# Kernel optimization log

Hardware: AMD Instinct MI355X
Metric: run time of the kernel (lower is better)

The kernel has to match this reference:

```python
import jax, jax.numpy as jnp
import numpy as np

# ---- problem sizes ----
N_NEURONS = 1536
N_INPUTS = 768
BATCH = 32
T = 256
DT = 1.0  # ms per step
SURRGRAD_SCALE = 10.0

# ---- per-cell-type physiology (recurrent): 0=excitatory, 1=inhibitory ----
CELL_TAU_MEM = np.array([20.0, 10.0], np.float32)   # ms
CELL_THETA   = np.array([-50.0, -50.0], np.float32) # mV
CELL_URESET  = np.array([-65.0, -65.0], np.float32) # mV
CELL_EL      = np.array([-65.0, -65.0], np.float32) # mV
CELL_GL      = np.array([10.0, 10.0], np.float32)   # nS
CELL_TAUREF  = np.array([2.0, 1.0], np.float32)     # ms

# ---- synapse types: AMPA(pre=exc), NMDA(pre=exc), GABA_A(pre=inh) ----
SYN_CELL_ID   = np.array([0, 0, 1], np.int32)
SYN_TAU_RISE  = np.array([0.5, 2.0, 0.5], np.float32)
SYN_TAU_DECAY = np.array([2.0, 100.0, 5.0], np.float32)
SYN_EREV      = np.array([0.0, 0.0, -70.0], np.float32)
SYN_GBAR      = np.array([1.0, 0.5, 1.0], np.float32)

# ---- feedforward: single excitatory input type, single AMPA synapse ----
FF_TAU_RISE, FF_TAU_DECAY, FF_EREV, FF_GBAR = 0.5, 2.0, 0.0, 1.0


@jax.custom_vjp
def spike(v):
    # Heaviside spike with fast-sigmoid surrogate gradient
    return (v >= 0).astype(v.dtype)

def _spike_fwd(v):
    return spike(v), v

def _spike_bwd(v, g):
    return (g / (SURRGRAD_SCALE * jnp.abs(v) + 1.0) ** 2,)

spike.defvjp(_spike_fwd, _spike_bwd)


def setup_inputs() -> dict:
    key = jax.random.key(0)
    ks = jax.random.split(key, 6)
    input_spikes = (jax.random.uniform(ks[0], (BATCH, T, N_INPUTS)) < 0.05).astype(jnp.float32)
    weights = jax.random.normal(ks[1], (N_NEURONS, N_NEURONS), jnp.float32) * 0.05
    weights_FF = jax.random.normal(ks[2], (N_INPUTS, N_NEURONS), jnp.float32) * 0.05
    cell_type_indices = jax.random.randint(ks[3], (N_NEURONS,), 0, 2, jnp.int32)
    cell_type_indices_FF = jnp.zeros((N_INPUTS,), jnp.int32)
    scaling_factors = jax.random.uniform(ks[4], (2, 2), jnp.float32, 0.5, 1.5)
    scaling_factors_FF = jax.random.uniform(ks[5], (1, 2), jnp.float32, 0.5, 1.5)
    return {
        'input_spikes': input_spikes,
        'weights': weights,
        'weights_FF': weights_FF,
        'scaling_factors': scaling_factors,
        'scaling_factors_FF': scaling_factors_FF,
        'cell_type_indices': cell_type_indices,
        'cell_type_indices_FF': cell_type_indices_FF,
    }


def _simulate(input_spikes, weights, weights_FF, scaling_factors, scaling_factors_FF,
              cell_type_indices, cell_type_indices_FF):
    ct = cell_type_indices
    B = input_spikes.shape[0]

    # per-neuron physiology gathered by cell type
    tau_mem = jnp.asarray(CELL_TAU_MEM)[ct]
    theta = jnp.asarray(CELL_THETA)[ct]
    u_reset = jnp.asarray(CELL_URESET)[ct]
    e_l = jnp.asarray(CELL_EL)[ct]
    g_l = jnp.asarray(CELL_GL)[ct]
    ref_steps = jnp.asarray(CELL_TAUREF)[ct] / DT
    leak_coef = DT / (tau_mem * g_l)  # dt / C_m

    # effective weights: cell-type scaling + presynaptic synapse-type mask
    sf = scaling_factors[ct[:, None], ct[None, :]]            # (N, N)
    W = weights * sf
    pre_mask = (jnp.asarray(SYN_CELL_ID)[:, None] == ct[None, :]).astype(W.dtype)  # (S, N)
    Ws = W[None, :, :] * pre_mask[:, :, None]                  # (S, N, N)
    sfF = scaling_factors_FF[cell_type_indices_FF[:, None], ct[None, :]]
    WF = weights_FF * sfF                                      # (n_in, N)

    alpha_r = jnp.exp(-DT / jnp.asarray(SYN_TAU_RISE))[:, None, None]   # (S,1,1)
    alpha_d = jnp.exp(-DT / jnp.asarray(SYN_TAU_DECAY))[:, None, None]
    arF = jnp.exp(jnp.float32(-DT / FF_TAU_RISE))
    adF = jnp.exp(jnp.float32(-DT / FF_TAU_DECAY))
    gbar = jnp.asarray(SYN_GBAR)
    gbarE = jnp.asarray(SYN_GBAR * SYN_EREV)
    S = gbar.shape[0]

    U0 = jnp.broadcast_to(e_l, (B, N_NEURONS))
    carry0 = (U0,
              jnp.zeros((B, N_NEURONS), jnp.float32),       # previous spikes
              jnp.zeros((S, B, N_NEURONS), jnp.float32),    # x (rise)
              jnp.zeros((S, B, N_NEURONS), jnp.float32),    # g (decay)
              jnp.zeros((B, N_NEURONS), jnp.float32),       # x_FF
              jnp.zeros((B, N_NEURONS), jnp.float32),       # g_FF
              jnp.zeros((B, N_NEURONS), jnp.float32))       # refractory counter

    def step(carry, I_t):
        U, s_prev, x, g, xF, gF, ref = carry
        # dual-exponential conductance update per synapse type
        inp = jnp.einsum('bn,snm->sbm', s_prev, Ws)
        x = alpha_r * x + inp
        g = alpha_d * g + x
        xF = arF * xF + I_t @ WF
        gF = adF * gF + xF
        # conductance-based synaptic current: sum_s gbar_s * g_s * (E_s - U)
        gtot = jnp.einsum('s,sbn->bn', gbar, g) + FF_GBAR * gF
        gE = jnp.einsum('s,sbn->bn', gbarE, g) + (FF_GBAR * FF_EREV) * gF
        I_syn = gE - gtot * U
        # leaky membrane integration
        U_new = U + leak_coef * (g_l * (e_l - U) + I_syn)
        # refractory clamp
        in_ref = ref > 0
        U_new = jnp.where(in_ref, u_reset, U_new)
        ref = jnp.maximum(ref - 1.0, 0.0)
        # surrogate-gradient spike and reset
        s_new = spike(U_new - theta)
        U_out = jnp.where(s_new > 0, u_reset, U_new)
        ref = jnp.where(s_new > 0, ref_steps, ref)
        return (U_out, s_new, x, g, xF, gF, ref), (s_new, U_out)

    I_seq = jnp.transpose(input_spikes, (1, 0, 2))  # (T, B, n_in)
    _, (spk, volts) = jax.lax.scan(step, carry0, I_seq)
    return jnp.transpose(spk, (1, 0, 2)), jnp.transpose(volts, (1, 0, 2))


def reference(input_spikes, weights, weights_FF, scaling_factors, scaling_factors_FF,
              cell_type_indices, cell_type_indices_FF):
    return _simulate(input_spikes, weights, weights_FF, scaling_factors, scaling_factors_FF,
                     cell_type_indices, cell_type_indices_FF)
```

## Files before the change

### kernel.cpp

```cpp
#include <hip/hip_runtime.h>
#include <stdint.h>


__global__ __launch_bounds__(768) void snn_lif_kernel(
    const float* __restrict__ I,
    const float* __restrict__ W,
    const float* __restrict__ WF,
    const float* __restrict__ sf,
    const float* __restrict__ sfF,
    const int*   __restrict__ ct,
    float* __restrict__ out,
    uint64_t* __restrict__ recpub)
{
    const int tid = threadIdx.x;
    const int j   = blockIdx.x & 7;
    const int b   = blockIdx.x >> 3;
    const int wv  = tid >> 6;
    const int wl  = tid & 63;

    __shared__ uint32_t ent[3840];
    __shared__ float    partF[11][192];
    __shared__ float    part0[12][192];
    __shared__ float    part1[12][192];
    __shared__ uint32_t totals_sh;
    __shared__ uint32_t tF_sh;
    __shared__ uint32_t ctm32_sh[48];
    __shared__ uint64_t fmask_sh[12];

    for (int r = 0; r < 2; ++r) {
        int c = ct[r * 768 + tid];
        uint64_t bal = __ballot(c != 0);
        if (wl == 0) {
            ctm32_sh[r * 24 + wv * 2]     = (uint32_t)bal;
            ctm32_sh[r * 24 + wv * 2 + 1] = (uint32_t)(bal >> 32);
        }
    }
    __syncthreads();

    const int m = j * 192 + ((tid < 192) ? tid : 0);
    const int   myct = ct[m];
    const float s0m  = sf[myct];
    const float s1m  = sf[2 + myct];
    const float sFm  = sfF[myct];
    const float lc   = (myct == 0) ? (1.0f / 200.0f) : (1.0f / 100.0f);
    const float refsteps = (myct == 0) ? 2.0f : 1.0f;
    const float ar0 = expf(-1.0f / 0.5f),  ad0 = expf(-1.0f / 2.0f);
    const float ar1 = expf(-1.0f / 2.0f),  ad1 = expf(-1.0f / 100.0f);
    const float ar2 = expf(-1.0f / 0.5f),  ad2 = expf(-1.0f / 5.0f);
    const float arF = expf(-1.0f / 0.5f),  adF = expf(-1.0f / 2.0f);

    float U = -65.0f, refc = 0.0f;
    float x0 = 0, g0 = 0, x1 = 0, g1 = 0, x2 = 0, g2 = 0, xF = 0, gF = 0;

    const uint32_t ctw = (wl < 48) ? ctm32_sh[wl] : 0u;
    const int btbase = b * 256;
    const uint32_t colv = (uint32_t)(j * 48 + wl);

    {
        float iv0 = __builtin_nontemporal_load(&I[(uint32_t)btbase * 768u + (uint32_t)tid]);
        uint64_t fb = __ballot(iv0 > 0.5f);
        if (wl == 0) fmask_sh[wv] = fb;
    }
    __syncthreads();
    if (wv == 0) {
        uint64_t fm = 0; uint32_t cF = 0;
        if (wl < 12) { fm = fmask_sh[wl]; cF = __popcll(fm); }
        uint32_t incl = cF;
        #pragma unroll
        for (int d = 1; d < 64; d <<= 1) {
            uint32_t u = __shfl_up(incl, d, 64);
            if (wl >= d) incl += u;
        }
        if (wl == 11) tF_sh = incl;
        if (wl < 12) {
            uint32_t pF = 3072u + (incl - cF);
            const uint32_t lanebase = (uint32_t)wl * 64u * 1536u;
            while (fm) {
                const int bit = __builtin_ctzll(fm);
                fm &= fm - 1;
                ent[pF++] = lanebase + (uint32_t)bit * 1536u;
            }
        }
    }

    for (int t = 0; t < 256; ++t) {
        __syncthreads();

        float iv_next = 0.0f;
        if (t < 255)
            iv_next = __builtin_nontemporal_load(
                &I[(uint32_t)(btbase + t + 1) * 768u + (uint32_t)tid]);

        if (wv == 0) {
            uint32_t sm = 0;
            if (wl < 48 && t > 0) {
                const uint32_t fi = (uint32_t)(btbase + t - 1) * 48u + (uint32_t)wl;
                for (;;) {
                    uint64_t v = __hip_atomic_load(&recpub[fi], __ATOMIC_RELAXED,
                                                   __HIP_MEMORY_SCOPE_AGENT);
                    if ((uint32_t)(v >> 32) == (uint32_t)t) { sm = (uint32_t)v; break; }
                    __builtin_amdgcn_s_sleep(1);
                }
            }
            const uint32_t c0 = __popc(sm & ~ctw);
            const uint32_t c1 = __popc(sm & ctw);
            uint32_t pack = c0 | (c1 << 16);
            uint32_t incl = pack;
            #pragma unroll
            for (int d = 1; d < 64; d <<= 1) {
                uint32_t u = __shfl_up(incl, d, 64);
                if (wl >= d) incl += u;
            }
            const uint32_t excl = incl - pack;
            if (wl == 47) totals_sh = incl;
            if (wl < 48) {
                uint32_t p0 = excl & 0xFFFFu;
                uint32_t p1 = 1536u + (excl >> 16);
                uint32_t mm = sm;
                const uint32_t lanebase = (uint32_t)wl * 32u * 1536u;
                while (mm) {
                    const int bit = __builtin_ctz(mm);
                    mm &= mm - 1;
                    const uint32_t off = lanebase + (uint32_t)bit * 1536u;
                    if ((ctw >> bit) & 1u) ent[p1++] = off;
                    else                   ent[p0++] = off;
                }
            }
        } else if (wl < 48) {
            const uint32_t tF = tF_sh;
            float4 zF = make_float4(0.f, 0.f, 0.f, 0.f);
            #pragma unroll 4
            for (uint32_t i = (uint32_t)(wv - 1); i < tF; i += 11u) {
                const float4 w = ((const float4*)(WF + ent[3072u + i]))[colv];
                zF.x += w.x; zF.y += w.y; zF.z += w.z; zF.w += w.w;
            }
            *(float4*)&partF[wv - 1][wl * 4] = zF;
        }
        __syncthreads();

        const uint32_t tp = totals_sh;
        const uint32_t t0 = tp & 0xFFFFu;
        const uint32_t t1 = tp >> 16;
        if (wl < 48) {
            float4 z0 = make_float4(0.f, 0.f, 0.f, 0.f);
            float4 z1 = z0;
            #pragma unroll 8
            for (uint32_t i = (uint32_t)wv; i < t0; i += 12u) {
                const float4 w = ((const float4*)(W + ent[i]))[colv];
                z0.x += w.x; z0.y += w.y; z0.z += w.z; z0.w += w.w;
            }
            #pragma unroll 8
            for (uint32_t i = (uint32_t)wv; i < t1; i += 12u) {
                const float4 w = ((const float4*)(W + ent[1536u + i]))[colv];
                z1.x += w.x; z1.y += w.y; z1.z += w.z; z1.w += w.w;
            }
            *(float4*)&part0[wv][wl * 4] = z0;
            *(float4*)&part1[wv][wl * 4] = z1;
        }
        {
            uint64_t fb = __ballot(iv_next > 0.5f);
            if (wl == 0) fmask_sh[wv] = fb;
        }
        __syncthreads();

        if (tid < 192) {
            float z0s = 0.f, z1s = 0.f, zFs = 0.f;
            #pragma unroll
            for (int k = 0; k < 11; ++k) zFs += partF[k][tid];
            #pragma unroll
            for (int k = 0; k < 12; ++k) { z0s += part0[k][tid]; z1s += part1[k][tid]; }
            z0s *= s0m; z1s *= s1m; zFs *= sFm;
            x0 = ar0 * x0 + z0s;  g0 = ad0 * g0 + x0;
            x1 = ar1 * x1 + z0s;  g1 = ad1 * g1 + x1;
            x2 = ar2 * x2 + z1s;  g2 = ad2 * g2 + x2;
            xF = arF * xF + zFs;  gF = adF * gF + xF;
            const float gtot = g0 + 0.5f * g1 + g2 + gF;
            const float gE   = -70.0f * g2;
            const float Isyn = gE - gtot * U;
            float Un = U + lc * (10.0f * (-65.0f - U) + Isyn);
            if (refc > 0.0f) Un = -65.0f;
            refc = fmaxf(refc - 1.0f, 0.0f);
            const bool s = (Un - (-50.0f)) >= 0.0f;
            const uint64_t bal = __ballot(s);
            if (wl == 0 || wl == 32) {
                const uint32_t half = (wl == 0) ? (uint32_t)bal : (uint32_t)(bal >> 32);
                const uint32_t word = (uint32_t)(j * 6 + wv * 2) + (wl == 32 ? 1u : 0u);
                const uint32_t widx = (uint32_t)(btbase + t) * 48u + word;
                const uint64_t v = ((uint64_t)(uint32_t)(t + 1) << 32) | half;
                __hip_atomic_store(&recpub[widx], v, __ATOMIC_RELAXED,
                                   __HIP_MEMORY_SCOPE_AGENT);
            }
            const float Uo = s ? -65.0f : Un;
            refc = s ? refsteps : refc;
            U = Uo;
            const uint32_t oidx = (uint32_t)(btbase + t) * 1536u + (uint32_t)m;
            __builtin_nontemporal_store(s ? 1.0f : 0.0f, &out[oidx]);
            __builtin_nontemporal_store(Uo, &out[12582912u + oidx]);
        }
        if (wv == 0 && t < 255) {
            uint64_t fm = 0; uint32_t cF = 0;
            if (wl < 12) { fm = fmask_sh[wl]; cF = __popcll(fm); }
            uint32_t incl = cF;
            #pragma unroll
            for (int d = 1; d < 64; d <<= 1) {
                uint32_t u = __shfl_up(incl, d, 64);
                if (wl >= d) incl += u;
            }
            if (wl == 11) tF_sh = incl;
            if (wl < 12) {
                uint32_t pF = 3072u + (incl - cF);
                const uint32_t lanebase = (uint32_t)wl * 64u * 1536u;
                while (fm) {
                    const int bit = __builtin_ctzll(fm);
                    fm &= fm - 1;
                    ent[pF++] = lanebase + (uint32_t)bit * 1536u;
                }
            }
        }
    }
}

extern "C" void kernel_launch(void* const* d_in, const int* in_sizes, int n_in,
                              void* d_out, int out_size, void* d_ws, size_t ws_size,
                              hipStream_t stream) {
    const float* I   = (const float*)d_in[0];
    const float* W   = (const float*)d_in[1];
    const float* WF  = (const float*)d_in[2];
    const float* sf  = (const float*)d_in[3];
    const float* sfF = (const float*)d_in[4];
    const int*   ct  = (const int*)d_in[5];

    uint64_t* recpub = (uint64_t*)d_ws;

    snn_lif_kernel<<<dim3(256), dim3(768), 0, stream>>>(
        I, W, WF, sf, sfF, ct, (float*)d_out, recpub);
}
```

Measured before the change: 845.3 us.

## Split each batch across 16 blocks of 384 threads with 96 neurons each

Each block now owns 96 neurons instead of 192, so the launch grows to 512 blocks of 384 threads. Each wave splits into two 24-lane half-rows that take alternating sparse-entry phases. The block-to-(batch, slice) mapping interleaves the two halves of a batch across blockIdx ranges. The intent is to shorten per-step gather and accumulate work and to use more CUs for the latency-bound recurrent loop. The cost is twice as many blocks polling the cross-block spike flags, duplicated per-block spike list construction, and more blocks that must be co-resident for the spin-wait scheme to avoid deadlock.

```diff
diff --git a/kernel.cpp b/kernel.cpp
--- a/kernel.cpp
+++ b/kernel.cpp
@@ -2,7 +2,7 @@
 #include <stdint.h>
 
 
-__global__ __launch_bounds__(768) void snn_lif_kernel(
+__global__ __launch_bounds__(384) void snn_lif_kernel(
     const float* __restrict__ I,
     const float* __restrict__ W,
     const float* __restrict__ WF,
@@ -13,31 +13,34 @@
     uint64_t* __restrict__ recpub)
 {
     const int tid = threadIdx.x;
-    const int j   = blockIdx.x & 7;
-    const int b   = blockIdx.x >> 3;
+    const int x    = blockIdx.x & 7;
+    const int r    = blockIdx.x >> 3;
+    const int half = r >> 5;
+    const int j    = x + 8 * half;
+    const int b    = ((r & 31) + (half << 4)) & 31;
     const int wv  = tid >> 6;
     const int wl  = tid & 63;
 
     __shared__ uint32_t ent[3840];
-    __shared__ float    partF[11][192];
-    __shared__ float    part0[12][192];
-    __shared__ float    part1[12][192];
+    __shared__ float    partF[10][96];
+    __shared__ float    part0[12][96];
+    __shared__ float    part1[12][96];
     __shared__ uint32_t totals_sh;
     __shared__ uint32_t tF_sh;
     __shared__ uint32_t ctm32_sh[48];
     __shared__ uint64_t fmask_sh[12];
 
-    for (int r = 0; r < 2; ++r) {
-        int c = ct[r * 768 + tid];
+    for (int rr = 0; rr < 4; ++rr) {
+        int c = ct[rr * 384 + tid];
         uint64_t bal = __ballot(c != 0);
         if (wl == 0) {
-            ctm32_sh[r * 24 + wv * 2]     = (uint32_t)bal;
-            ctm32_sh[r * 24 + wv * 2 + 1] = (uint32_t)(bal >> 32);
+            ctm32_sh[rr * 12 + wv * 2]     = (uint32_t)bal;
+            ctm32_sh[rr * 12 + wv * 2 + 1] = (uint32_t)(bal >> 32);
         }
     }
     __syncthreads();
 
-    const int m = j * 192 + ((tid < 192) ? tid : 0);
+    const int m = j * 96 + ((tid < 96) ? tid : 0);
     const int   myct = ct[m];
     const float s0m  = sf[myct];
     const float s1m  = sf[2 + myct];
@@ -54,12 +57,15 @@
 
     const uint32_t ctw = (wl < 48) ? ctm32_sh[wl] : 0u;
     const int btbase = b * 256;
-    const uint32_t colv = (uint32_t)(j * 48 + wl);
+    const int row_sub = (wl >= 24) ? 1 : 0;
+    const uint32_t colv4 = (uint32_t)(j * 24 + (wl - row_sub * 24));
 
     {
-        float iv0 = __builtin_nontemporal_load(&I[(uint32_t)btbase * 768u + (uint32_t)tid]);
-        uint64_t fb = __ballot(iv0 > 0.5f);
-        if (wl == 0) fmask_sh[wv] = fb;
+        float iva = __builtin_nontemporal_load(&I[(uint32_t)btbase * 768u + (uint32_t)tid]);
+        float ivb = __builtin_nontemporal_load(&I[(uint32_t)btbase * 768u + 384u + (uint32_t)tid]);
+        uint64_t fa = __ballot(iva > 0.5f);
+        uint64_t fb = __ballot(ivb > 0.5f);
+        if (wl == 0) { fmask_sh[wv] = fa; fmask_sh[wv + 6] = fb; }
     }
     __syncthreads();
     if (wv == 0) {
@@ -86,10 +92,12 @@
     for (int t = 0; t < 256; ++t) {
         __syncthreads();
 
-        float iv_next = 0.0f;
-        if (t < 255)
-            iv_next = __builtin_nontemporal_load(
-                &I[(uint32_t)(btbase + t + 1) * 768u + (uint32_t)tid]);
+        float iva_n = 0.0f, ivb_n = 0.0f;
+        if (t < 255) {
+            const uint32_t base = (uint32_t)(btbase + t + 1) * 768u;
+            iva_n = __builtin_nontemporal_load(&I[base + (uint32_t)tid]);
+            ivb_n = __builtin_nontemporal_load(&I[base + 384u + (uint32_t)tid]);
+        }
 
         if (wv == 0) {
             uint32_t sm = 0;
@@ -128,13 +136,14 @@
             }
         } else if (wl < 48) {
             const uint32_t tF = tF_sh;
+            const uint32_t phase = (uint32_t)((wv - 1) * 2 + row_sub);
             float4 zF = make_float4(0.f, 0.f, 0.f, 0.f);
             #pragma unroll 4
-            for (uint32_t i = (uint32_t)(wv - 1); i < tF; i += 11u) {
-                const float4 w = ((const float4*)(WF + ent[3072u + i]))[colv];
+            for (uint32_t i = phase; i < tF; i += 10u) {
+                const float4 w = ((const float4*)(WF + ent[3072u + i]))[colv4];
                 zF.x += w.x; zF.y += w.y; zF.z += w.z; zF.w += w.w;
             }
-            *(float4*)&partF[wv - 1][wl * 4] = zF;
+            *(float4*)&partF[phase][(wl - row_sub * 24) * 4] = zF;
         }
         __syncthreads();
 
@@ -142,31 +151,34 @@
         const uint32_t t0 = tp & 0xFFFFu;
         const uint32_t t1 = tp >> 16;
         if (wl < 48) {
+            const uint32_t phase = (uint32_t)(wv * 2 + row_sub);
             float4 z0 = make_float4(0.f, 0.f, 0.f, 0.f);
             float4 z1 = z0;
-            #pragma unroll 8
-            for (uint32_t i = (uint32_t)wv; i < t0; i += 12u) {
-                const float4 w = ((const float4*)(W + ent[i]))[colv];
+            #pragma unroll 4
+            for (uint32_t i = phase; i < t0; i += 12u) {
+                const float4 w = ((const float4*)(W + ent[i]))[colv4];
                 z0.x += w.x; z0.y += w.y; z0.z += w.z; z0.w += w.w;
             }
-            #pragma unroll 8
-            for (uint32_t i = (uint32_t)wv; i < t1; i += 12u) {
-                const float4 w = ((const float4*)(W + ent[1536u + i]))[colv];
+            #pragma unroll 4
+            for (uint32_t i = phase; i < t1; i += 12u) {
+                const float4 w = ((const float4*)(W + ent[1536u + i]))[colv4];
                 z1.x += w.x; z1.y += w.y; z1.z += w.z; z1.w += w.w;
             }
-            *(float4*)&part0[wv][wl * 4] = z0;
-            *(float4*)&part1[wv][wl * 4] = z1;
+            const int c4 = (wl - row_sub * 24) * 4;
+            *(float4*)&part0[phase][c4] = z0;
+            *(float4*)&part1[phase][c4] = z1;
         }
         {
-            uint64_t fb = __ballot(iv_next > 0.5f);
-            if (wl == 0) fmask_sh[wv] = fb;
+            uint64_t fa = __ballot(iva_n > 0.5f);
+            uint64_t fb = __ballot(ivb_n > 0.5f);
+            if (wl == 0) { fmask_sh[wv] = fa; fmask_sh[wv + 6] = fb; }
         }
         __syncthreads();
 
-        if (tid < 192) {
+        if (tid < 96) {
             float z0s = 0.f, z1s = 0.f, zFs = 0.f;
             #pragma unroll
-            for (int k = 0; k < 11; ++k) zFs += partF[k][tid];
+            for (int k = 0; k < 10; ++k) zFs += partF[k][tid];
             #pragma unroll
             for (int k = 0; k < 12; ++k) { z0s += part0[k][tid]; z1s += part1[k][tid]; }
             z0s *= s0m; z1s *= s1m; zFs *= sFm;
@@ -182,11 +194,11 @@
             refc = fmaxf(refc - 1.0f, 0.0f);
             const bool s = (Un - (-50.0f)) >= 0.0f;
             const uint64_t bal = __ballot(s);
-            if (wl == 0 || wl == 32) {
-                const uint32_t half = (wl == 0) ? (uint32_t)bal : (uint32_t)(bal >> 32);
-                const uint32_t word = (uint32_t)(j * 6 + wv * 2) + (wl == 32 ? 1u : 0u);
-                const uint32_t widx = (uint32_t)(btbase + t) * 48u + word;
-                const uint64_t v = ((uint64_t)(uint32_t)(t + 1) << 32) | half;
+            if (wl == 0 || (wv == 0 && wl == 32)) {
+                const uint32_t wib  = (wv == 0) ? ((wl == 32) ? 1u : 0u) : 2u;
+                const uint32_t bits = (wl == 32) ? (uint32_t)(bal >> 32) : (uint32_t)bal;
+                const uint32_t widx = (uint32_t)(btbase + t) * 48u + (uint32_t)(j * 3) + wib;
+                const uint64_t v = ((uint64_t)(uint32_t)(t + 1) << 32) | bits;
                 __hip_atomic_store(&recpub[widx], v, __ATOMIC_RELAXED,
                                    __HIP_MEMORY_SCOPE_AGENT);
             }
@@ -232,6 +244,6 @@
 
     uint64_t* recpub = (uint64_t*)d_ws;
 
-    snn_lif_kernel<<<dim3(256), dim3(768), 0, stream>>>(
+    snn_lif_kernel<<<dim3(512), dim3(384), 0, stream>>>(
         I, W, WF, sf, sfF, ct, (float*)d_out, recpub);
 }
```

Measured after the change: 839.2 us. Within noise of the previous version (-0.7%).
